# Kernel tuning notes

Hardware: AMD Instinct MI355X
Metric: run time of the kernel (lower is better)

Reference implementation:

```python
import jax, jax.numpy as jnp
import numpy as np

B, T, D, H, FF = 4, 2048, 768, 12, 4
DH = D // H


def _ln(x, g, b, eps=1e-5):
    mu = x.mean(-1, keepdims=True)
    var = ((x - mu) ** 2).mean(-1, keepdims=True)
    return (x - mu) * jax.lax.rsqrt(var + eps) * g + b


def setup_inputs() -> dict:
    key = jax.random.key(0)
    ks = jax.random.split(key, 16)
    s = 0.02
    d = {
        'x': jax.random.normal(ks[0], (B, T, D), jnp.float32),
        'Wq': jax.random.normal(ks[1], (D, D), jnp.float32) * s,
        'bq': jnp.zeros((D,), jnp.float32),
        'Wk': jax.random.normal(ks[2], (D, D), jnp.float32) * s,
        'bk': jnp.zeros((D,), jnp.float32),
        'Wv': jax.random.normal(ks[3], (D, D), jnp.float32) * s,
        'bv': jnp.zeros((D,), jnp.float32),
        'Wo': jax.random.normal(ks[4], (D, D), jnp.float32) * s,
        'bo': jnp.zeros((D,), jnp.float32),
        'W1': jax.random.normal(ks[5], (D, D * FF), jnp.float32) * s,
        'b1': jnp.zeros((D * FF,), jnp.float32),
        'W2': jax.random.normal(ks[6], (D * FF, D), jnp.float32) * s,
        'b2': jnp.zeros((D,), jnp.float32),
        'g1': jnp.ones((D,), jnp.float32),
        'be1': jnp.zeros((D,), jnp.float32),
        'g2': jnp.ones((D,), jnp.float32),
        'be2': jnp.zeros((D,), jnp.float32),
        'radius': 64,
    }
    return d


def reference(x, Wq, bq, Wk, bk, Wv, bv, Wo, bo, W1, b1, W2, b2, g1, be1, g2, be2, radius):
    Bc, Tc, Dc = x.shape
    # local mask: blocked (True) where |i-j| > radius (clamping in torch code is a no-op)
    i = jnp.arange(Tc)
    mask = jnp.abs(i[:, None] - i[None, :]) > radius  # [T,T] True = masked

    h = _ln(x, g1, be1)
    q = (h @ Wq + bq).reshape(Bc, Tc, H, DH)
    k = (h @ Wk + bk).reshape(Bc, Tc, H, DH)
    v = (h @ Wv + bv).reshape(Bc, Tc, H, DH)
    scale = 1.0 / jnp.sqrt(jnp.asarray(DH, x.dtype))
    scores = jnp.einsum('bthd,bshd->bhts', q, k) * scale  # [B,H,T,T]
    scores = jnp.where(mask[None, None], -jnp.inf, scores)
    attn = jax.nn.softmax(scores, axis=-1)
    ctx = jnp.einsum('bhts,bshd->bthd', attn, v).reshape(Bc, Tc, Dc)
    x = x + (ctx @ Wo + bo)

    h2 = _ln(x, g2, be2)
    ff = jax.nn.gelu(h2 @ W1 + b1, approximate=False) @ W2 + b2
    return x + ff
```

## Files before the change

kernel.cpp:

```cpp
#include <hip/hip_runtime.h>
#include <hip/hip_bf16.h>

#define B_  4
#define T_  2048
#define D_  768
#define H_  12
#define DH_ 64
#define FF_ 3072

typedef __attribute__((ext_vector_type(8))) short bf16x8;
typedef __attribute__((ext_vector_type(4))) float f32x4;
typedef __attribute__((ext_vector_type(4))) unsigned short us4;

#define MFMA16(a, b, c) __builtin_amdgcn_mfma_f32_16x16x32_bf16((a), (b), (c), 0, 0, 0)

__device__ __forceinline__ unsigned short f2bf(float f) {
    union { float f; unsigned u; } v; v.f = f;
    unsigned r = v.u + 0x7fffu + ((v.u >> 16) & 1u);
    return (unsigned short)(r >> 16);
}

__device__ __forceinline__ void gload_lds16(const unsigned short* gp, unsigned short* lp) {
    __builtin_amdgcn_global_load_lds(
        (const __attribute__((address_space(1))) unsigned int*)gp,
        (__attribute__((address_space(3))) unsigned int*)lp,
        16, 0, 0);
}

__global__ __launch_bounds__(256) void tcvt_kernel(
    const float* __restrict__ src, unsigned short* __restrict__ dst, int K, int N)
{
    __shared__ float tile[32][33];
    const int bx = blockIdx.x * 32;
    const int by = blockIdx.y * 32;
    const int tx = threadIdx.x, ty = threadIdx.y;
#pragma unroll
    for (int i = 0; i < 32; i += 8)
        tile[ty + i][tx] = src[(size_t)(by + ty + i) * N + bx + tx];
    __syncthreads();
#pragma unroll
    for (int i = 0; i < 32; i += 8)
        dst[(size_t)(bx + ty + i) * K + by + tx] = f2bf(tile[tx][ty + i]);
}

__global__ __launch_bounds__(256) void tcvt4_kernel(
    const float* __restrict__ s0, const float* __restrict__ s1,
    const float* __restrict__ s2, const float* __restrict__ s3,
    unsigned short* __restrict__ dst)
{
    __shared__ float tile[32][33];
    const int z = blockIdx.z;
    const float* src = (z == 0) ? s0 : (z == 1) ? s1 : (z == 2) ? s2 : s3;
    unsigned short* d = dst + (size_t)z * 589824;
    const int bx = blockIdx.x * 32;
    const int by = blockIdx.y * 32;
    const int tx = threadIdx.x, ty = threadIdx.y;
#pragma unroll
    for (int i = 0; i < 32; i += 8)
        tile[ty + i][tx] = src[(size_t)(by + ty + i) * 768 + bx + tx];
    __syncthreads();
#pragma unroll
    for (int i = 0; i < 32; i += 8)
        d[(size_t)(bx + ty + i) * 768 + by + tx] = f2bf(tile[tx][ty + i]);
}

__global__ __launch_bounds__(256) void ln_kernel(
    const float* __restrict__ x, const float* __restrict__ g,
    const float* __restrict__ be, unsigned short* __restrict__ out)
{
    const int row = blockIdx.x;
    const int t = threadIdx.x;
    const float* xr = x + (size_t)row * D_;
    float v0 = xr[t], v1 = xr[t + 256], v2 = xr[t + 512];
    float s = v0 + v1 + v2;
    float s2 = v0 * v0 + v1 * v1 + v2 * v2;
#pragma unroll
    for (int o = 1; o < 64; o <<= 1) {
        s  += __shfl_xor(s,  o);
        s2 += __shfl_xor(s2, o);
    }
    __shared__ float rs[4], rq[4];
    const int wave = t >> 6;
    if ((t & 63) == 0) { rs[wave] = s; rq[wave] = s2; }
    __syncthreads();
    s  = rs[0] + rs[1] + rs[2] + rs[3];
    s2 = rq[0] + rq[1] + rq[2] + rq[3];
    const float mu = s * (1.0f / D_);
    const float var = s2 * (1.0f / D_) - mu * mu;
    const float rstd = rsqrtf(var + 1e-5f);
    unsigned short* orow = out + (size_t)row * D_;
    orow[t]       = f2bf((v0 - mu) * rstd * g[t]       + be[t]);
    orow[t + 256] = f2bf((v1 - mu) * rstd * g[t + 256] + be[t + 256]);
    orow[t + 512] = f2bf((v2 - mu) * rstd * g[t + 512] + be[t + 512]);
}

template<int MODE>
__global__ __launch_bounds__(512) void gemm512(
    const unsigned short* __restrict__ A,
    const unsigned short* __restrict__ Bt,
    const float* __restrict__ bias,
    const float* __restrict__ bias2,
    const float* __restrict__ bias3,
    const float* __restrict__ resid,
    void* __restrict__ outp,
    void* __restrict__ out2,
    void* __restrict__ out3,
    int N, int K, int nTilesN)
{
    __shared__ __align__(16) unsigned short As[128 * 64];
    __shared__ __align__(16) unsigned short Bs[128 * 64];

    const int nwg = gridDim.x;
    const int q = nwg >> 3, rr = nwg & 7;
    const int xcd = blockIdx.x & 7, loc = blockIdx.x >> 3;
    const int swz = (xcd < rr ? xcd * (q + 1) : rr * (q + 1) + (xcd - rr) * q) + loc;
    const int m0 = (swz / nTilesN) * 128;
    const int n0 = (swz % nTilesN) * 128;

    const int tid = threadIdx.x;
    const int wv = tid >> 6;
    const int lane = tid & 63;
    const int wr = wv >> 1;
    const int wc = wv & 1;

    f32x4 zero4 = {0.0f, 0.0f, 0.0f, 0.0f};
    f32x4 acc[2][4];
#pragma unroll
    for (int i = 0; i < 2; ++i)
#pragma unroll
        for (int j = 0; j < 4; ++j) acc[i][j] = zero4;

    const int lrow = lane >> 3;
    const int scb = (lane & 7) ^ lrow;
    const size_t ag0 = (size_t)(m0 + wv * 16 + lrow) * K + scb * 8;
    const size_t ag1 = ag0 + (size_t)8 * K;
    const size_t bg0 = (size_t)(n0 + wv * 16 + lrow) * K + scb * 8;
    const size_t bg1 = bg0 + (size_t)8 * K;
    unsigned short* AsW = As + wv * 1024;
    unsigned short* BsW = Bs + wv * 1024;

    const int fr = lane & 15;
    const int fg = lane >> 4;
    const int sw = fr & 7;

    const int nk = K >> 6;
    for (int kt = 0; kt < nk; ++kt) {
        const int k0 = kt << 6;
        __syncthreads();
        gload_lds16(A  + ag0 + k0, AsW);
        gload_lds16(A  + ag1 + k0, AsW + 512);
        gload_lds16(Bt + bg0 + k0, BsW);
        gload_lds16(Bt + bg1 + k0, BsW + 512);
        __syncthreads();
#pragma unroll
        for (int kk = 0; kk < 2; ++kk) {
            bf16x8 afr[2], bfr[4];
#pragma unroll
            for (int mm = 0; mm < 2; ++mm) {
                const int row = wr * 32 + mm * 16 + fr;
                afr[mm] = *(const bf16x8*)(As + row * 64 + (((kk * 4 + fg) ^ sw) << 3));
            }
#pragma unroll
            for (int nn = 0; nn < 4; ++nn) {
                const int row = wc * 64 + nn * 16 + fr;
                bfr[nn] = *(const bf16x8*)(Bs + row * 64 + (((kk * 4 + fg) ^ sw) << 3));
            }
#pragma unroll
            for (int mm = 0; mm < 2; ++mm)
#pragma unroll
                for (int nn = 0; nn < 4; ++nn)
                    acc[mm][nn] = MFMA16(afr[mm], bfr[nn], acc[mm][nn]);
        }
    }

    const int lc = lane & 15;
    const int lr = (lane >> 4) * 4;
#pragma unroll
    for (int mm = 0; mm < 2; ++mm) {
        const int gm0 = m0 + wr * 32 + mm * 16 + lr;
#pragma unroll
        for (int nn = 0; nn < 4; ++nn) {
            const int gn = n0 + wc * 64 + nn * 16 + lc;
            if (MODE == 4) {
                if (gn < 1536) {
                    const float bv = (gn < 768) ? bias[gn] : bias2[gn - 768];
                    unsigned short* o = (gn < 768) ? (unsigned short*)outp : (unsigned short*)out2;
                    const int col = (gn < 768) ? gn : gn - 768;
#pragma unroll
                    for (int r = 0; r < 4; ++r)
                        o[(size_t)(gm0 + r) * 768 + col] = f2bf(acc[mm][nn][r] + bv);
                } else {
                    const float bv = bias3[gn - 1536];
                    const int b = gm0 / T_;
                    const int tl = gm0 - b * T_;
                    us4 pk;
#pragma unroll
                    for (int r = 0; r < 4; ++r) pk[r] = f2bf(acc[mm][nn][r] + bv);
                    *(us4*)((unsigned short*)out3 + ((size_t)(b * D_ + gn - 1536)) * T_ + tl) = pk;
                }
            } else {
                const float bv = bias[gn];
#pragma unroll
                for (int r = 0; r < 4; ++r) {
                    const int gm = gm0 + r;
                    float v = acc[mm][nn][r] + bv;
                    if (MODE == 0) {
                        ((unsigned short*)outp)[(size_t)gm * N + gn] = f2bf(v);
                    } else if (MODE == 2) {
                        v = 0.5f * v * (1.0f + erff(v * 0.70710678118654752f));
                        ((unsigned short*)outp)[(size_t)gm * N + gn] = f2bf(v);
                    } else if (MODE == 3) {
                        ((float*)outp)[(size_t)gm * N + gn] = v + resid[(size_t)gm * N + gn];
                    }
                }
            }
        }
    }
}

__global__ __launch_bounds__(256) void attn_kernel(
    const unsigned short* __restrict__ Q,
    const unsigned short* __restrict__ Kg,
    const unsigned short* __restrict__ Vt,
    unsigned short* __restrict__ ctx)
{
    __shared__ __align__(16) unsigned short Qs[64][72];
    __shared__ __align__(16) unsigned short KP[192 * 72];
    __shared__ __align__(16) unsigned short Vts[64][200];

    const int tid = threadIdx.x;
    const int lane = tid & 63;
    const int w = tid >> 6;
    const int bid = blockIdx.x;
    const int qt = bid & 31;
    const int h = (bid >> 5) % H_;
    const int b = bid / (32 * H_);
    const int qs = qt * 64;
    const int t0 = qs >= 64 ? qs - 64 : 0;
    const int t1 = (qs + 128 < T_) ? qs + 128 : T_;
    const int KW = t1 - t0;

    for (int s = tid; s < 512; s += 256) {
        const int r = s >> 3, c8 = (s & 7) << 3;
        *(uint4*)&Qs[r][c8] =
            *(const uint4*)&Q[((size_t)(b * T_ + qs + r)) * D_ + h * DH_ + c8];
    }
    unsigned short* Ks = KP;
    for (int s = tid; s < 1536; s += 256) {
        const int r = s >> 3, c8 = (s & 7) << 3;
        uint4 val = {0, 0, 0, 0};
        if (r < KW)
            val = *(const uint4*)&Kg[((size_t)(b * T_ + t0 + r)) * D_ + h * DH_ + c8];
        *(uint4*)&Ks[r * 72 + c8] = val;
    }
    for (int s = tid; s < 1536; s += 256) {
        const int r = s / 24, c8 = (s % 24) << 3;
        uint4 val = {0, 0, 0, 0};
        if (c8 < KW)
            val = *(const uint4*)&Vt[((size_t)((b * H_ + h) * DH_ + r)) * T_ + t0 + c8];
        *(uint4*)&Vts[r][c8] = val;
    }
    __syncthreads();

    f32x4 zero4 = {0.0f, 0.0f, 0.0f, 0.0f};
    f32x4 sa[12];
#pragma unroll
    for (int i = 0; i < 12; ++i) sa[i] = zero4;
#pragma unroll
    for (int ks = 0; ks < 2; ++ks) {
        const bf16x8 aq = *(const bf16x8*)&Qs[w * 16 + (lane & 15)][ks * 32 + (lane >> 4) * 8];
#pragma unroll
        for (int cf = 0; cf < 12; ++cf) {
            const bf16x8 bk = *(const bf16x8*)&Ks[(cf * 16 + (lane & 15)) * 72 + ks * 32 + (lane >> 4) * 8];
            sa[cf] = MFMA16(aq, bk, sa[cf]);
        }
    }
    __syncthreads();

    const int lq = w * 16 + (lane >> 4) * 4;
    float mx[4] = {-1e30f, -1e30f, -1e30f, -1e30f};
#pragma unroll
    for (int cf = 0; cf < 12; ++cf) {
        const int key = t0 + cf * 16 + (lane & 15);
#pragma unroll
        for (int r = 0; r < 4; ++r) {
            const int dd = (qs + lq + r) - key;
            const bool ok = (key < t1) && (dd <= 64) && (dd >= -64);
            const float sv = ok ? sa[cf][r] * 0.125f : -1e30f;
            sa[cf][r] = sv;
            mx[r] = fmaxf(mx[r], sv);
        }
    }
#pragma unroll
    for (int r = 0; r < 4; ++r)
#pragma unroll
        for (int o = 1; o < 16; o <<= 1)
            mx[r] = fmaxf(mx[r], __shfl_xor(mx[r], o));

    unsigned short* Ps = KP;
    float sm[4] = {0.0f, 0.0f, 0.0f, 0.0f};
#pragma unroll
    for (int cf = 0; cf < 12; ++cf) {
#pragma unroll
        for (int r = 0; r < 4; ++r) {
            const float p = __expf(sa[cf][r] - mx[r]);
            sm[r] += p;
            Ps[(lq + r) * 200 + cf * 16 + (lane & 15)] = f2bf(p);
        }
    }
#pragma unroll
    for (int r = 0; r < 4; ++r)
#pragma unroll
        for (int o = 1; o < 16; o <<= 1)
            sm[r] += __shfl_xor(sm[r], o);

    f32x4 oa[4];
#pragma unroll
    for (int i = 0; i < 4; ++i) oa[i] = zero4;
#pragma unroll
    for (int ks = 0; ks < 6; ++ks) {
        const bf16x8 ap = *(const bf16x8*)&Ps[(w * 16 + (lane & 15)) * 200 + ks * 32 + (lane >> 4) * 8];
#pragma unroll
        for (int nf = 0; nf < 4; ++nf) {
            const bf16x8 bv = *(const bf16x8*)&Vts[nf * 16 + (lane & 15)][ks * 32 + (lane >> 4) * 8];
            oa[nf] = MFMA16(ap, bv, oa[nf]);
        }
    }
#pragma unroll
    for (int nf = 0; nf < 4; ++nf) {
#pragma unroll
        for (int r = 0; r < 4; ++r) {
            const float o = oa[nf][r] / sm[r];
            ctx[((size_t)(b * T_ + qs + lq + r)) * D_ + h * DH_ + nf * 16 + (lane & 15)] = f2bf(o);
        }
    }
}

extern "C" void kernel_launch(void* const* d_in, const int* in_sizes, int n_in,
                              void* d_out, int out_size, void* d_ws, size_t ws_size,
                              hipStream_t stream)
{
    const float* x   = (const float*)d_in[0];
    const float* Wq  = (const float*)d_in[1];
    const float* bq  = (const float*)d_in[2];
    const float* Wk  = (const float*)d_in[3];
    const float* bk  = (const float*)d_in[4];
    const float* Wv  = (const float*)d_in[5];
    const float* bv  = (const float*)d_in[6];
    const float* Wo  = (const float*)d_in[7];
    const float* bo  = (const float*)d_in[8];
    const float* W1  = (const float*)d_in[9];
    const float* b1  = (const float*)d_in[10];
    const float* W2  = (const float*)d_in[11];
    const float* b2  = (const float*)d_in[12];
    const float* g1  = (const float*)d_in[13];
    const float* be1 = (const float*)d_in[14];
    const float* g2  = (const float*)d_in[15];
    const float* be2 = (const float*)d_in[16];
    float* out = (float*)d_out;

    unsigned short* wqkv_t = (unsigned short*)d_ws;
    unsigned short* wo_t = wqkv_t + 3 * 589824;
    unsigned short* w1_t = wo_t + 589824;
    unsigned short* w2_t = w1_t + 2359296;
    unsigned short* hbuf = w2_t + 2359296;
    unsigned short* qbuf = hbuf + 6291456;
    float* x2 = (float*)(qbuf + 6291456);
    unsigned short* kbuf = (unsigned short*)(x2 + 6291456);
    unsigned short* vtb  = kbuf + 6291456;
    unsigned short* ffb  = kbuf;

    dim3 tb(32, 8);
    tcvt4_kernel<<<dim3(24, 24, 4), tb, 0, stream>>>(Wq, Wk, Wv, Wo, wqkv_t);
    tcvt_kernel<<<dim3(96, 24), tb, 0, stream>>>(W1, w1_t, 768, 3072);
    tcvt_kernel<<<dim3(24, 96), tb, 0, stream>>>(W2, w2_t, 3072, 768);

    ln_kernel<<<8192, 256, 0, stream>>>(x, g1, be1, hbuf);

    gemm512<4><<<64 * 18, 512, 0, stream>>>(
        hbuf, wqkv_t, bq, bk, bv, nullptr, qbuf, kbuf, vtb, 2304, 768, 18);

    attn_kernel<<<1536, 256, 0, stream>>>(qbuf, kbuf, vtb, hbuf);

    gemm512<3><<<64 * 6, 512, 0, stream>>>(
        hbuf, wo_t, bo, nullptr, nullptr, x, x2, nullptr, nullptr, 768, 768, 6);

    ln_kernel<<<8192, 256, 0, stream>>>(x2, g2, be2, qbuf);

    gemm512<2><<<64 * 24, 512, 0, stream>>>(
        qbuf, w1_t, b1, nullptr, nullptr, nullptr, ffb, nullptr, nullptr, 3072, 768, 24);

    gemm512<3><<<64 * 6, 512, 0, stream>>>(
        ffb, w2_t, b2, nullptr, nullptr, x2, out, nullptr, nullptr, 768, 3072, 6);
}
```

Measured before the change: 232.9 us.

## Triple-buffer GEMM LDS tiles with prefetch two K-steps ahead

The GEMM main loop moves from a single LDS buffer with two barriers per K-step to a three-stage ring in dynamic shared memory. Global-to-LDS loads are issued two tiles ahead, and waits use explicit vmcnt counts so only one barrier per step remains. Fragment loads are batched before the MFMA block, which runs at raised wave priority. LDS use per block grows to 96 KB, which may limit occupancy to one 512-thread block per CU.

```diff
diff --git a/kernel.cpp b/kernel.cpp
--- a/kernel.cpp
+++ b/kernel.cpp
@@ -107,8 +107,7 @@
     void* __restrict__ out3,
     int N, int K, int nTilesN)
 {
-    __shared__ __align__(16) unsigned short As[128 * 64];
-    __shared__ __align__(16) unsigned short Bs[128 * 64];
+    extern __shared__ __align__(16) unsigned short lds[];
 
     const int nwg = gridDim.x;
     const int q = nwg >> 3, rr = nwg & 7;
@@ -136,41 +135,73 @@
     const size_t ag1 = ag0 + (size_t)8 * K;
     const size_t bg0 = (size_t)(n0 + wv * 16 + lrow) * K + scb * 8;
     const size_t bg1 = bg0 + (size_t)8 * K;
-    unsigned short* AsW = As + wv * 1024;
-    unsigned short* BsW = Bs + wv * 1024;
+    const int woff = wv * 1024;
 
     const int fr = lane & 15;
     const int fg = lane >> 4;
     const int sw = fr & 7;
 
+    unsigned short* pc = lds;
+    unsigned short* pn = lds + 16384;
+    unsigned short* ps = lds + 32768;
+
     const int nk = K >> 6;
-    for (int kt = 0; kt < nk; ++kt) {
-        const int k0 = kt << 6;
-        __syncthreads();
-        gload_lds16(A  + ag0 + k0, AsW);
-        gload_lds16(A  + ag1 + k0, AsW + 512);
-        gload_lds16(Bt + bg0 + k0, BsW);
-        gload_lds16(Bt + bg1 + k0, BsW + 512);
-        __syncthreads();
+
+    {
+        gload_lds16(A  + ag0, pc + woff);
+        gload_lds16(A  + ag1, pc + woff + 512);
+        gload_lds16(Bt + bg0, pc + 8192 + woff);
+        gload_lds16(Bt + bg1, pc + 8192 + woff + 512);
+        if (nk > 1) {
+            const int k0 = 64;
+            gload_lds16(A  + ag0 + k0, pn + woff);
+            gload_lds16(A  + ag1 + k0, pn + woff + 512);
+            gload_lds16(Bt + bg0 + k0, pn + 8192 + woff);
+            gload_lds16(Bt + bg1 + k0, pn + 8192 + woff + 512);
+        }
+    }
+
+    for (int t = 0; t < nk; ++t) {
+        if (t < nk - 1) asm volatile("s_waitcnt vmcnt(4)" ::: "memory");
+        else            asm volatile("s_waitcnt vmcnt(0)" ::: "memory");
+        __builtin_amdgcn_s_barrier();
+        asm volatile("" ::: "memory");
+
+        if (t + 2 < nk) {
+            const int k0 = (t + 2) << 6;
+            gload_lds16(A  + ag0 + k0, ps + woff);
+            gload_lds16(A  + ag1 + k0, ps + woff + 512);
+            gload_lds16(Bt + bg0 + k0, ps + 8192 + woff);
+            gload_lds16(Bt + bg1 + k0, ps + 8192 + woff + 512);
+        }
+
+        bf16x8 afr[2][2], bfr[2][4];
 #pragma unroll
         for (int kk = 0; kk < 2; ++kk) {
-            bf16x8 afr[2], bfr[4];
 #pragma unroll
             for (int mm = 0; mm < 2; ++mm) {
                 const int row = wr * 32 + mm * 16 + fr;
-                afr[mm] = *(const bf16x8*)(As + row * 64 + (((kk * 4 + fg) ^ sw) << 3));
+                afr[kk][mm] = *(const bf16x8*)(pc + row * 64 + (((kk * 4 + fg) ^ sw) << 3));
             }
 #pragma unroll
             for (int nn = 0; nn < 4; ++nn) {
                 const int row = wc * 64 + nn * 16 + fr;
-                bfr[nn] = *(const bf16x8*)(Bs + row * 64 + (((kk * 4 + fg) ^ sw) << 3));
+                bfr[kk][nn] = *(const bf16x8*)(pc + 8192 + row * 64 + (((kk * 4 + fg) ^ sw) << 3));
             }
+        }
+        asm volatile("s_waitcnt lgkmcnt(0)" ::: "memory");
+        __builtin_amdgcn_sched_barrier(0);
+        __builtin_amdgcn_s_setprio(1);
+#pragma unroll
+        for (int kk = 0; kk < 2; ++kk)
 #pragma unroll
             for (int mm = 0; mm < 2; ++mm)
 #pragma unroll
                 for (int nn = 0; nn < 4; ++nn)
-                    acc[mm][nn] = MFMA16(afr[mm], bfr[nn], acc[mm][nn]);
-        }
+                    acc[mm][nn] = MFMA16(afr[kk][mm], bfr[kk][nn], acc[mm][nn]);
+        __builtin_amdgcn_s_setprio(0);
+
+        unsigned short* tmp = pc; pc = pn; pn = ps; ps = tmp;
     }
 
     const int lc = lane & 15;
@@ -370,6 +401,8 @@
     unsigned short* vtb  = kbuf + 6291456;
     unsigned short* ffb  = kbuf;
 
+    const size_t gemm_lds = 3 * 32768;
+
     dim3 tb(32, 8);
     tcvt4_kernel<<<dim3(24, 24, 4), tb, 0, stream>>>(Wq, Wk, Wv, Wo, wqkv_t);
     tcvt_kernel<<<dim3(96, 24), tb, 0, stream>>>(W1, w1_t, 768, 3072);
@@ -377,19 +410,19 @@
 
     ln_kernel<<<8192, 256, 0, stream>>>(x, g1, be1, hbuf);
 
-    gemm512<4><<<64 * 18, 512, 0, stream>>>(
+    gemm512<4><<<64 * 18, 512, gemm_lds, stream>>>(
         hbuf, wqkv_t, bq, bk, bv, nullptr, qbuf, kbuf, vtb, 2304, 768, 18);
 
     attn_kernel<<<1536, 256, 0, stream>>>(qbuf, kbuf, vtb, hbuf);
 
-    gemm512<3><<<64 * 6, 512, 0, stream>>>(
+    gemm512<3><<<64 * 6, 512, gemm_lds, stream>>>(
         hbuf, wo_t, bo, nullptr, nullptr, x, x2, nullptr, nullptr, 768, 768, 6);
 
     ln_kernel<<<8192, 256, 0, stream>>>(x2, g2, be2, qbuf);
 
-    gemm512<2><<<64 * 24, 512, 0, stream>>>(
+    gemm512<2><<<64 * 24, 512, gemm_lds, stream>>>(
         qbuf, w1_t, b1, nullptr, nullptr, nullptr, ffb, nullptr, nullptr, 3072, 768, 24);
 
-    gemm512<3><<<64 * 6, 512, 0, stream>>>(
+    gemm512<3><<<64 * 6, 512, gemm_lds, stream>>>(
         ffb, w2_t, b2, nullptr, nullptr, x2, out, nullptr, nullptr, 768, 3072, 6);
 }
```

New measurement: 275.7 us. 18.4% more time.

## Rewrite GEMM as 256x128 tile with triple-buffered async LDS pipeline

Applied to the files above, without the earlier changes.

The GEMM kernel now uses 256x128 output tiles with 32-wide K steps, staged through a three-deep LDS ring buffer filled by direct global-to-LDS loads. Each K step is split into two MFMA phases interleaved with the next prefetches, using explicit waitcnt, barriers, and setprio. The aim is to hide global load latency and reuse the B fragments across more rows, in place of the old fully synchronous load-then-compute loop. The cost is more accumulator registers, 72KB of dynamic LDS per block, and half as many workgroups, which lowers occupancy and grid fill for the small N=768 GEMMs.

```diff
diff --git a/kernel.cpp b/kernel.cpp
--- a/kernel.cpp
+++ b/kernel.cpp
@@ -95,7 +95,7 @@
 }
 
 template<int MODE>
-__global__ __launch_bounds__(512) void gemm512(
+__global__ __launch_bounds__(512, 4) void gemm8p(
     const unsigned short* __restrict__ A,
     const unsigned short* __restrict__ Bt,
     const float* __restrict__ bias,
@@ -107,14 +107,13 @@
     void* __restrict__ out3,
     int N, int K, int nTilesN)
 {
-    __shared__ __align__(16) unsigned short As[128 * 64];
-    __shared__ __align__(16) unsigned short Bs[128 * 64];
+    extern __shared__ __align__(16) unsigned short lds[];
 
     const int nwg = gridDim.x;
     const int q = nwg >> 3, rr = nwg & 7;
     const int xcd = blockIdx.x & 7, loc = blockIdx.x >> 3;
     const int swz = (xcd < rr ? xcd * (q + 1) : rr * (q + 1) + (xcd - rr) * q) + loc;
-    const int m0 = (swz / nTilesN) * 128;
+    const int m0 = (swz / nTilesN) * 256;
     const int n0 = (swz % nTilesN) * 128;
 
     const int tid = threadIdx.x;
@@ -124,60 +123,91 @@
     const int wc = wv & 1;
 
     f32x4 zero4 = {0.0f, 0.0f, 0.0f, 0.0f};
-    f32x4 acc[2][4];
-#pragma unroll
-    for (int i = 0; i < 2; ++i)
+    f32x4 acc[4][4];
+#pragma unroll
+    for (int i = 0; i < 4; ++i)
 #pragma unroll
         for (int j = 0; j < 4; ++j) acc[i][j] = zero4;
 
-    const int lrow = lane >> 3;
-    const int scb = (lane & 7) ^ lrow;
-    const size_t ag0 = (size_t)(m0 + wv * 16 + lrow) * K + scb * 8;
-    const size_t ag1 = ag0 + (size_t)8 * K;
-    const size_t bg0 = (size_t)(n0 + wv * 16 + lrow) * K + scb * 8;
-    const size_t bg1 = bg0 + (size_t)8 * K;
-    unsigned short* AsW = As + wv * 1024;
-    unsigned short* BsW = Bs + wv * 1024;
+    const int lrow = lane >> 2;
+    const int skey = (lrow & 3) ^ ((lrow >> 2) & 3);
+    const int scb  = (lane & 3) ^ skey;
+    const unsigned short* pA0 = A  + (size_t)(m0 + wv * 32 + lrow) * K + scb * 8;
+    const unsigned short* pA1 = pA0 + (size_t)16 * K;
+    const unsigned short* pB  = Bt + (size_t)(n0 + wv * 16 + lrow) * K + scb * 8;
+    const int aD0 = wv * 32 * 32;
+    const int aD1 = aD0 + 16 * 32;
+    const int bD  = 8192 + wv * 16 * 32;
 
     const int fr = lane & 15;
     const int fg = lane >> 4;
-    const int sw = fr & 7;
-
-    const int nk = K >> 6;
-    for (int kt = 0; kt < nk; ++kt) {
-        const int k0 = kt << 6;
-        __syncthreads();
-        gload_lds16(A  + ag0 + k0, AsW);
-        gload_lds16(A  + ag1 + k0, AsW + 512);
-        gload_lds16(Bt + bg0 + k0, BsW);
-        gload_lds16(Bt + bg1 + k0, BsW + 512);
-        __syncthreads();
-#pragma unroll
-        for (int kk = 0; kk < 2; ++kk) {
-            bf16x8 afr[2], bfr[4];
-#pragma unroll
-            for (int mm = 0; mm < 2; ++mm) {
-                const int row = wr * 32 + mm * 16 + fr;
-                afr[mm] = *(const bf16x8*)(As + row * 64 + (((kk * 4 + fg) ^ sw) << 3));
-            }
-#pragma unroll
-            for (int nn = 0; nn < 4; ++nn) {
-                const int row = wc * 64 + nn * 16 + fr;
-                bfr[nn] = *(const bf16x8*)(Bs + row * 64 + (((kk * 4 + fg) ^ sw) << 3));
-            }
-#pragma unroll
-            for (int mm = 0; mm < 2; ++mm)
-#pragma unroll
-                for (int nn = 0; nn < 4; ++nn)
-                    acc[mm][nn] = MFMA16(afr[mm], bfr[nn], acc[mm][nn]);
-        }
+    const int rb = ((fg ^ (fr & 3) ^ ((fr >> 2) & 3)) << 3);
+    const int aOff = (wr * 64 + fr) * 32 + rb;
+    const int bOff = 8192 + (wc * 64 + fr) * 32 + rb;
+
+    unsigned short* pc = lds;
+    unsigned short* pn = lds + 12288;
+    unsigned short* ps = lds + 24576;
+
+    const int nk = K >> 5;
+
+    gload_lds16(pA0, pc + aD0); gload_lds16(pA1, pc + aD1); gload_lds16(pB, pc + bD);
+    pA0 += 32; pA1 += 32; pB += 32;
+    gload_lds16(pA0, pn + aD0); gload_lds16(pA1, pn + aD1); gload_lds16(pB, pn + bD);
+    pA0 += 32; pA1 += 32; pB += 32;
+    asm volatile("s_waitcnt vmcnt(3)" ::: "memory");
+    __builtin_amdgcn_s_barrier();
+
+    for (int t = 0; t < nk; ++t) {
+        const bool st = (t + 2 < nk);
+        bf16x8 a0 = *(const bf16x8*)(pc + aOff);
+        bf16x8 a1 = *(const bf16x8*)(pc + aOff + 512);
+        bf16x8 b0 = *(const bf16x8*)(pc + bOff);
+        bf16x8 b1 = *(const bf16x8*)(pc + bOff + 512);
+        bf16x8 b2 = *(const bf16x8*)(pc + bOff + 1024);
+        bf16x8 b3 = *(const bf16x8*)(pc + bOff + 1536);
+        if (st) { gload_lds16(pA0, ps + aD0); gload_lds16(pA1, ps + aD1); }
+        asm volatile("s_waitcnt lgkmcnt(0)" ::: "memory");
+        __builtin_amdgcn_sched_barrier(0);
+        __builtin_amdgcn_s_setprio(1);
+        acc[0][0] = MFMA16(a0, b0, acc[0][0]);
+        acc[0][1] = MFMA16(a0, b1, acc[0][1]);
+        acc[0][2] = MFMA16(a0, b2, acc[0][2]);
+        acc[0][3] = MFMA16(a0, b3, acc[0][3]);
+        acc[1][0] = MFMA16(a1, b0, acc[1][0]);
+        acc[1][1] = MFMA16(a1, b1, acc[1][1]);
+        acc[1][2] = MFMA16(a1, b2, acc[1][2]);
+        acc[1][3] = MFMA16(a1, b3, acc[1][3]);
+        __builtin_amdgcn_s_setprio(0);
+        __builtin_amdgcn_s_barrier();
+
+        bf16x8 a2 = *(const bf16x8*)(pc + aOff + 1024);
+        bf16x8 a3 = *(const bf16x8*)(pc + aOff + 1536);
+        if (st) { gload_lds16(pB, ps + bD); pA0 += 32; pA1 += 32; pB += 32; }
+        asm volatile("s_waitcnt lgkmcnt(0)" ::: "memory");
+        __builtin_amdgcn_sched_barrier(0);
+        __builtin_amdgcn_s_setprio(1);
+        acc[2][0] = MFMA16(a2, b0, acc[2][0]);
+        acc[2][1] = MFMA16(a2, b1, acc[2][1]);
+        acc[2][2] = MFMA16(a2, b2, acc[2][2]);
+        acc[2][3] = MFMA16(a2, b3, acc[2][3]);
+        acc[3][0] = MFMA16(a3, b0, acc[3][0]);
+        acc[3][1] = MFMA16(a3, b1, acc[3][1]);
+        acc[3][2] = MFMA16(a3, b2, acc[3][2]);
+        acc[3][3] = MFMA16(a3, b3, acc[3][3]);
+        __builtin_amdgcn_s_setprio(0);
+        if (st)               asm volatile("s_waitcnt vmcnt(3)" ::: "memory");
+        else if (t + 1 < nk)  asm volatile("s_waitcnt vmcnt(0)" ::: "memory");
+        __builtin_amdgcn_s_barrier();
+
+        unsigned short* tmp = pc; pc = pn; pn = ps; ps = tmp;
     }
 
     const int lc = lane & 15;
     const int lr = (lane >> 4) * 4;
 #pragma unroll
-    for (int mm = 0; mm < 2; ++mm) {
-        const int gm0 = m0 + wr * 32 + mm * 16 + lr;
+    for (int mm = 0; mm < 4; ++mm) {
+        const int gm0 = m0 + wr * 64 + mm * 16 + lr;
 #pragma unroll
         for (int nn = 0; nn < 4; ++nn) {
             const int gn = n0 + wc * 64 + nn * 16 + lc;
@@ -370,6 +400,8 @@
     unsigned short* vtb  = kbuf + 6291456;
     unsigned short* ffb  = kbuf;
 
+    const size_t gemm_lds = 3 * 24576;
+
     dim3 tb(32, 8);
     tcvt4_kernel<<<dim3(24, 24, 4), tb, 0, stream>>>(Wq, Wk, Wv, Wo, wqkv_t);
     tcvt_kernel<<<dim3(96, 24), tb, 0, stream>>>(W1, w1_t, 768, 3072);
@@ -377,19 +409,19 @@
 
     ln_kernel<<<8192, 256, 0, stream>>>(x, g1, be1, hbuf);
 
-    gemm512<4><<<64 * 18, 512, 0, stream>>>(
+    gemm8p<4><<<32 * 18, 512, gemm_lds, stream>>>(
         hbuf, wqkv_t, bq, bk, bv, nullptr, qbuf, kbuf, vtb, 2304, 768, 18);
 
     attn_kernel<<<1536, 256, 0, stream>>>(qbuf, kbuf, vtb, hbuf);
 
-    gemm512<3><<<64 * 6, 512, 0, stream>>>(
+    gemm8p<3><<<32 * 6, 512, gemm_lds, stream>>>(
         hbuf, wo_t, bo, nullptr, nullptr, x, x2, nullptr, nullptr, 768, 768, 6);
 
     ln_kernel<<<8192, 256, 0, stream>>>(x2, g2, be2, qbuf);
 
-    gemm512<2><<<64 * 24, 512, 0, stream>>>(
+    gemm8p<2><<<32 * 24, 512, gemm_lds, stream>>>(
         qbuf, w1_t, b1, nullptr, nullptr, nullptr, ffb, nullptr, nullptr, 3072, 768, 24);
 
-    gemm512<3><<<64 * 6, 512, 0, stream>>>(
+    gemm8p<3><<<32 * 6, 512, gemm_lds, stream>>>(
         ffb, w2_t, b2, nullptr, nullptr, x2, out, nullptr, nullptr, 768, 3072, 6);
 }
```

Result: slower. 257.6 us (+10.6%).

## Template GEMM on wave count with 64x64 per-wave tiles and taller M tiles

Applied to the files above, without the earlier changes.

The GEMM kernel becomes a template over wave count, and each wave now computes a 64x64 output sub-tile (4x4 MFMA fragments) instead of 32x64. This raises MFMA work per LDS fragment load. The QKV and FF1 GEMMs use 4-wave 128x128 blocks. The Wo and FF2 GEMMs use 8-wave 256x128 blocks with half as many workgroups. The larger per-wave tiles raise register pressure, and halving the grid for the N=768 GEMMs can leave CUs idle (192 workgroups on 256 CUs).

```diff
diff --git a/kernel.cpp b/kernel.cpp
--- a/kernel.cpp
+++ b/kernel.cpp
@@ -94,8 +94,8 @@
     orow[t + 512] = f2bf((v2 - mu) * rstd * g[t + 512] + be[t + 512]);
 }
 
-template<int MODE>
-__global__ __launch_bounds__(512) void gemm512(
+template<int MODE, int WAVES>
+__global__ __launch_bounds__(WAVES * 64, (WAVES == 4) ? 3 : 2) void gemmK(
     const unsigned short* __restrict__ A,
     const unsigned short* __restrict__ Bt,
     const float* __restrict__ bias,
@@ -107,14 +107,15 @@
     void* __restrict__ out3,
     int N, int K, int nTilesN)
 {
-    __shared__ __align__(16) unsigned short As[128 * 64];
+    constexpr int BM = (WAVES == 4) ? 128 : 256;
+    __shared__ __align__(16) unsigned short As[BM * 64];
     __shared__ __align__(16) unsigned short Bs[128 * 64];
 
     const int nwg = gridDim.x;
     const int q = nwg >> 3, rr = nwg & 7;
     const int xcd = blockIdx.x & 7, loc = blockIdx.x >> 3;
     const int swz = (xcd < rr ? xcd * (q + 1) : rr * (q + 1) + (xcd - rr) * q) + loc;
-    const int m0 = (swz / nTilesN) * 128;
+    const int m0 = (swz / nTilesN) * BM;
     const int n0 = (swz % nTilesN) * 128;
 
     const int tid = threadIdx.x;
@@ -124,49 +125,51 @@
     const int wc = wv & 1;
 
     f32x4 zero4 = {0.0f, 0.0f, 0.0f, 0.0f};
-    f32x4 acc[2][4];
-#pragma unroll
-    for (int i = 0; i < 2; ++i)
+    f32x4 acc[4][4];
+#pragma unroll
+    for (int i = 0; i < 4; ++i)
 #pragma unroll
         for (int j = 0; j < 4; ++j) acc[i][j] = zero4;
 
+    constexpr int ACH = BM / WAVES / 8;
+    constexpr int BCH = 128 / WAVES / 8;
     const int lrow = lane >> 3;
     const int scb = (lane & 7) ^ lrow;
-    const size_t ag0 = (size_t)(m0 + wv * 16 + lrow) * K + scb * 8;
-    const size_t ag1 = ag0 + (size_t)8 * K;
-    const size_t bg0 = (size_t)(n0 + wv * 16 + lrow) * K + scb * 8;
-    const size_t bg1 = bg0 + (size_t)8 * K;
-    unsigned short* AsW = As + wv * 1024;
-    unsigned short* BsW = Bs + wv * 1024;
+    const unsigned short* ag = A + (size_t)(m0 + wv * (BM / WAVES) + lrow) * K + scb * 8;
+    const unsigned short* bg = Bt + (size_t)(n0 + wv * (128 / WAVES) + lrow) * K + scb * 8;
+    unsigned short* aLds = As + wv * (BM / WAVES) * 64;
+    unsigned short* bLds = Bs + wv * (128 / WAVES) * 64;
 
     const int fr = lane & 15;
     const int fg = lane >> 4;
     const int sw = fr & 7;
+    const int aRow = (wr * 64 + fr) * 64;
+    const int bRow = (wc * 64 + fr) * 64;
 
     const int nk = K >> 6;
     for (int kt = 0; kt < nk; ++kt) {
         const int k0 = kt << 6;
         __syncthreads();
-        gload_lds16(A  + ag0 + k0, AsW);
-        gload_lds16(A  + ag1 + k0, AsW + 512);
-        gload_lds16(Bt + bg0 + k0, BsW);
-        gload_lds16(Bt + bg1 + k0, BsW + 512);
+#pragma unroll
+        for (int c = 0; c < ACH; ++c)
+            gload_lds16(ag + k0 + (size_t)c * 8 * K, aLds + c * 512);
+#pragma unroll
+        for (int c = 0; c < BCH; ++c)
+            gload_lds16(bg + k0 + (size_t)c * 8 * K, bLds + c * 512);
         __syncthreads();
+
 #pragma unroll
         for (int kk = 0; kk < 2; ++kk) {
-            bf16x8 afr[2], bfr[4];
-#pragma unroll
-            for (int mm = 0; mm < 2; ++mm) {
-                const int row = wr * 32 + mm * 16 + fr;
-                afr[mm] = *(const bf16x8*)(As + row * 64 + (((kk * 4 + fg) ^ sw) << 3));
-            }
-#pragma unroll
-            for (int nn = 0; nn < 4; ++nn) {
-                const int row = wc * 64 + nn * 16 + fr;
-                bfr[nn] = *(const bf16x8*)(Bs + row * 64 + (((kk * 4 + fg) ^ sw) << 3));
-            }
-#pragma unroll
-            for (int mm = 0; mm < 2; ++mm)
+            bf16x8 afr[4], bfr[4];
+            const int cb = ((kk * 4 + fg) ^ sw) << 3;
+#pragma unroll
+            for (int mm = 0; mm < 4; ++mm)
+                afr[mm] = *(const bf16x8*)(As + aRow + mm * 1024 + cb);
+#pragma unroll
+            for (int nn = 0; nn < 4; ++nn)
+                bfr[nn] = *(const bf16x8*)(Bs + bRow + nn * 1024 + cb);
+#pragma unroll
+            for (int mm = 0; mm < 4; ++mm)
 #pragma unroll
                 for (int nn = 0; nn < 4; ++nn)
                     acc[mm][nn] = MFMA16(afr[mm], bfr[nn], acc[mm][nn]);
@@ -176,8 +179,8 @@
     const int lc = lane & 15;
     const int lr = (lane >> 4) * 4;
 #pragma unroll
-    for (int mm = 0; mm < 2; ++mm) {
-        const int gm0 = m0 + wr * 32 + mm * 16 + lr;
+    for (int mm = 0; mm < 4; ++mm) {
+        const int gm0 = m0 + wr * 64 + mm * 16 + lr;
 #pragma unroll
         for (int nn = 0; nn < 4; ++nn) {
             const int gn = n0 + wc * 64 + nn * 16 + lc;
@@ -377,19 +380,19 @@
 
     ln_kernel<<<8192, 256, 0, stream>>>(x, g1, be1, hbuf);
 
-    gemm512<4><<<64 * 18, 512, 0, stream>>>(
+    gemmK<4, 4><<<64 * 18, 256, 0, stream>>>(
         hbuf, wqkv_t, bq, bk, bv, nullptr, qbuf, kbuf, vtb, 2304, 768, 18);
 
     attn_kernel<<<1536, 256, 0, stream>>>(qbuf, kbuf, vtb, hbuf);
 
-    gemm512<3><<<64 * 6, 512, 0, stream>>>(
+    gemmK<3, 8><<<32 * 6, 512, 0, stream>>>(
         hbuf, wo_t, bo, nullptr, nullptr, x, x2, nullptr, nullptr, 768, 768, 6);
 
     ln_kernel<<<8192, 256, 0, stream>>>(x2, g2, be2, qbuf);
 
-    gemm512<2><<<64 * 24, 512, 0, stream>>>(
+    gemmK<2, 4><<<64 * 24, 256, 0, stream>>>(
         qbuf, w1_t, b1, nullptr, nullptr, nullptr, ffb, nullptr, nullptr, 3072, 768, 24);
 
-    gemm512<3><<<64 * 6, 512, 0, stream>>>(
+    gemmK<3, 8><<<32 * 6, 512, 0, stream>>>(
         ffb, w2_t, b2, nullptr, nullptr, x2, out, nullptr, nullptr, 768, 3072, 6);
 }
```

Result: slower. 261.5 us (+12.3%).
